# Performance work log

Measured on AMD Instinct MI355X. Metric: run time of the kernel, lower is better.

The kernel has to match this reference:

```python
import jax, jax.numpy as jnp
import numpy as np

S, D, M, K, H = 4096, 768, 1024, 32, 8
DH = D // H  # 96
CTX = 10
EPS_LN = 1e-5
EPS_COS = 1e-8


def setup_inputs() -> dict:
    key = jax.random.key(0)
    ks = jax.random.split(key, 30)
    sc = 0.02
    n = lambda k, shp: jax.random.normal(k, shp, jnp.float32) * sc
    inp = {
        "text_embeddings": jax.random.normal(ks[0], (1, S, D), jnp.float32),
        "candidate_embeddings": jax.random.normal(ks[1], (M, K, D), jnp.float32),
        "mention_starts": jax.random.randint(ks[2], (M,), 0, S - 16),
        "span_lengths": jax.random.randint(ks[3], (M,), 0, 8),
        # relik_reader: Linear(2D->D), ReLU, Linear(D->1)
        "relik_w1": n(ks[4], (2 * D, D)), "relik_b1": jnp.zeros((D,), jnp.float32),
        "relik_w2": n(ks[5], (D, 1)), "relik_b2": jnp.zeros((1,), jnp.float32),
        # TransformerEncoderLayer (post-norm, relu, nhead=8, ffn=4D)
        "wq": n(ks[6], (D, D)), "bq": jnp.zeros((D,), jnp.float32),
        "wk": n(ks[7], (D, D)), "bk": jnp.zeros((D,), jnp.float32),
        "wv": n(ks[8], (D, D)), "bv": jnp.zeros((D,), jnp.float32),
        "wo": n(ks[9], (D, D)), "bo": jnp.zeros((D,), jnp.float32),
        "ln1_g": jnp.ones((D,), jnp.float32), "ln1_b": jnp.zeros((D,), jnp.float32),
        "ffn_w1": n(ks[10], (D, 4 * D)), "ffn_b1": jnp.zeros((4 * D,), jnp.float32),
        "ffn_w2": n(ks[11], (4 * D, D)), "ffn_b2": jnp.zeros((D,), jnp.float32),
        "ln2_g": jnp.ones((D,), jnp.float32), "ln2_b": jnp.zeros((D,), jnp.float32),
        # unirel_interaction: Linear(2D->D), ReLU, Linear(D->D)
        "uni_w1": n(ks[12], (2 * D, D)), "uni_b1": jnp.zeros((D,), jnp.float32),
        "uni_w2": n(ks[13], (D, D)), "uni_b2": jnp.zeros((D,), jnp.float32),
    }
    return inp


def _ln(x, g, b):
    mu = jnp.mean(x, -1, keepdims=True)
    var = jnp.mean(jnp.square(x - mu), -1, keepdims=True)
    return (x - mu) * jax.lax.rsqrt(var + EPS_LN) * g + b


def reference(text_embeddings, candidate_embeddings, mention_starts, span_lengths,
              relik_w1, relik_b1, relik_w2, relik_b2,
              wq, bq, wk, bk, wv, bv, wo, bo,
              ln1_g, ln1_b, ffn_w1, ffn_b1, ffn_w2, ffn_b2, ln2_g, ln2_b,
              uni_w1, uni_b1, uni_w2, uni_b2):
    txt = text_embeddings[0]                               # [S, D]
    seq = txt.shape[0]
    csum = jnp.concatenate([jnp.zeros((1, txt.shape[1]), txt.dtype),
                            jnp.cumsum(txt, axis=0)], axis=0)  # [S+1, D]
    ends = mention_starts + span_lengths
    # mean over [start, end] inclusive
    m_len = (span_lengths + 1).astype(txt.dtype)
    mention = (csum[ends + 1] - csum[mention_starts]) / m_len[:, None]  # [M, D]
    # context mean over [c_start, c_end) exclusive, as in original slicing
    c_start = jnp.maximum(0, mention_starts - CTX)
    c_end = jnp.minimum(seq - 1, ends + CTX)
    ctx = (csum[c_end] - csum[c_start]) / (c_end - c_start).astype(txt.dtype)[:, None]

    cand = candidate_embeddings                            # [M, K, D]
    mk = jnp.broadcast_to(mention[:, None, :], cand.shape) # [M, K, D]

    # relik score: MLP on [mention; candidate]
    cat_mc = jnp.concatenate([mk, cand], axis=-1)          # [M, K, 2D]
    h = jax.nn.relu(cat_mc @ relik_w1 + relik_b1)
    relik = (h @ relik_w2 + relik_b2)[..., 0]              # [M, K]

    # 2-token transformer encoder layer over stack([mention, candidate])
    x = jnp.stack([mk, cand], axis=2)                      # [M, K, 2, D]
    q = (x @ wq + bq).reshape(M, K, 2, H, DH)
    k_ = (x @ wk + bk).reshape(M, K, 2, H, DH)
    v = (x @ wv + bv).reshape(M, K, 2, H, DH)
    scores = jnp.einsum("mkqhd,mkvhd->mkhqv", q, k_) / jnp.sqrt(jnp.float32(DH))
    attn = jax.nn.softmax(scores, axis=-1)
    o = jnp.einsum("mkhqv,mkvhd->mkqhd", attn, v).reshape(M, K, 2, D)
    x1 = _ln(x + (o @ wo + bo), ln1_g, ln1_b)
    f = jax.nn.relu(x1 @ ffn_w1 + ffn_b1) @ ffn_w2 + ffn_b2
    x2 = _ln(x1 + f, ln2_g, ln2_b)                         # [M, K, 2, D]
    e0, e1 = x2[..., 0, :], x2[..., 1, :]
    n0 = jnp.maximum(jnp.linalg.norm(e0, axis=-1), EPS_COS)
    n1 = jnp.maximum(jnp.linalg.norm(e1, axis=-1), EPS_COS)
    atg = jnp.sum(e0 * e1, axis=-1) / (n0 * n1)            # [M, K]

    # unirel: MLP on [context; candidate], sigmoid of mean
    ck = jnp.broadcast_to(ctx[:, None, :], cand.shape)
    cat_cc = jnp.concatenate([ck, cand], axis=-1)
    inter = jax.nn.relu(cat_cc @ uni_w1 + uni_b1) @ uni_w2 + uni_b2
    unirel = jax.nn.sigmoid(jnp.mean(inter, axis=-1))      # [M, K]

    return jnp.stack([relik, atg, unirel], axis=0)         # [3, M, K]
```

## Files before the change

### kernel.cpp

```cpp
#include <hip/hip_runtime.h>
#include <math.h>

#define S_LEN 4096
#define D_DIM 768
#define M_CNT 1024
#define K_CNT 32
#define MK_CNT 32768
#define DH_DIM 96
#define CTX_W 10

typedef __bf16 bf16_t;
typedef bf16_t bf16x8 __attribute__((ext_vector_type(8)));
typedef float f32x4 __attribute__((ext_vector_type(4)));
typedef float f32x16 __attribute__((ext_vector_type(16)));
typedef int i32x4 __attribute__((ext_vector_type(4)));
typedef int i32x8 __attribute__((ext_vector_type(8)));

__device__ __forceinline__ float block_reduce_sum(float v, float* sbuf) {
#pragma unroll
    for (int off = 32; off; off >>= 1) v += __shfl_down(v, off);
    __syncthreads();
    int wave = threadIdx.x >> 6;
    int lane = threadIdx.x & 63;
    if (lane == 0) sbuf[wave] = v;
    __syncthreads();
    return sbuf[0] + sbuf[1] + sbuf[2] + sbuf[3];
}

__device__ __forceinline__ float wave_sum(float v) {
#pragma unroll
    for (int off = 32; off; off >>= 1) v += __shfl_down(v, off);
    return __shfl(v, 0);
}

__device__ __forceinline__ unsigned char to_fp8(float v) {
    return (unsigned char)(__builtin_amdgcn_cvt_pk_fp8_f32(v, v, 0, false) & 0xff);
}

template<int OUT_BF16, int RELU>
__global__ __launch_bounds__(256, 2) void gemm_mfma(
    const bf16_t* __restrict__ A, const bf16_t* __restrict__ Bt,
    const float* __restrict__ bias, void* __restrict__ C,
    int Kd, int N, int nx, int ny)
{
    __shared__ bf16_t As[128 * 64];
    __shared__ bf16_t Bs[128 * 64];
    const int tid = threadIdx.x;
    const int w = tid >> 6, l = tid & 63;
    int per = 8 * nx;
    int g = blockIdx.x / per, rr = blockIdx.x % per;
    int gs = ny - g * 8; if (gs > 8) gs = 8;
    const int row0 = (g * 8 + rr % gs) * 128, col0 = (rr / gs) * 128;

    const int srow = w * 8 + (l >> 3);
    const int gchunk = (l & 7) ^ ((l >> 3) & 7);
    const bf16_t* gA = A + (size_t)(row0 + srow) * Kd + gchunk * 8;
    const bf16_t* gB = Bt + (size_t)(col0 + srow) * Kd + gchunk * 8;

    const int wm = w >> 1, wn = w & 1;
    f32x4 acc[4][4] = {};

    for (int k0 = 0; k0 < Kd; k0 += 64) {
#pragma unroll
        for (int c = 0; c < 4; ++c) {
            __builtin_amdgcn_global_load_lds(
                (const __attribute__((address_space(1))) void*)(gA + (size_t)(c * 32) * Kd + k0),
                (__attribute__((address_space(3))) void*)(As + (c * 256 + w * 64) * 8), 16, 0, 0);
            __builtin_amdgcn_global_load_lds(
                (const __attribute__((address_space(1))) void*)(gB + (size_t)(c * 32) * Kd + k0),
                (__attribute__((address_space(3))) void*)(Bs + (c * 256 + w * 64) * 8), 16, 0, 0);
        }
        __syncthreads();
#pragma unroll
        for (int ks = 0; ks < 2; ++ks) {
            bf16x8 af[4], bfr[4];
#pragma unroll
            for (int i = 0; i < 4; ++i) {
                int arow = wm * 64 + i * 16 + (l & 15);
                int slot = (ks * 4 + (l >> 4)) ^ (l & 7);
                af[i] = *(const bf16x8*)(As + arow * 64 + slot * 8);
                int brow = wn * 64 + i * 16 + (l & 15);
                bfr[i] = *(const bf16x8*)(Bs + brow * 64 + slot * 8);
            }
#pragma unroll
            for (int i = 0; i < 4; ++i)
#pragma unroll
                for (int j = 0; j < 4; ++j)
                    acc[i][j] = __builtin_amdgcn_mfma_f32_16x16x32_bf16(af[i], bfr[j], acc[i][j], 0, 0, 0);
        }
        __syncthreads();
    }

#pragma unroll
    for (int i = 0; i < 4; ++i) {
        int row = row0 + wm * 64 + i * 16 + (l >> 4) * 4;
#pragma unroll
        for (int j = 0; j < 4; ++j) {
            int col = col0 + wn * 64 + j * 16 + (l & 15);
            float bv = bias ? bias[col] : 0.f;
#pragma unroll
            for (int r = 0; r < 4; ++r) {
                float v = acc[i][j][r] + bv;
                if (RELU) v = fmaxf(v, 0.f);
                if (OUT_BF16) ((bf16_t*)C)[(size_t)(row + r) * N + col] = (bf16_t)v;
                else          ((float*)C)[(size_t)(row + r) * N + col] = v;
            }
        }
    }
}

static inline void launch_gemm(const bf16_t* A, const bf16_t* Bt, const float* bias, void* C,
                               int rows, int Kd, int N, bool relu, bool outbf, hipStream_t st) {
    int nx = N / 128, ny = rows / 128;
    dim3 grid(nx * ny);
    if (outbf) {
        if (relu) gemm_mfma<1, 1><<<grid, 256, 0, st>>>(A, Bt, bias, C, Kd, N, nx, ny);
        else      gemm_mfma<1, 0><<<grid, 256, 0, st>>>(A, Bt, bias, C, Kd, N, nx, ny);
    } else {
        if (relu) gemm_mfma<0, 1><<<grid, 256, 0, st>>>(A, Bt, bias, C, Kd, N, nx, ny);
        else      gemm_mfma<0, 0><<<grid, 256, 0, st>>>(A, Bt, bias, C, Kd, N, nx, ny);
    }
}

template<int OMODE, int RELU, int RESID>
__global__ __launch_bounds__(256, 2) void gemm_fp8(
    const unsigned char* __restrict__ A, const unsigned char* __restrict__ Bt,
    const float* __restrict__ bias, void* __restrict__ C,
    const bf16_t* __restrict__ resid,
    int Kd, int N, int nx, int ny)
{
    __shared__ unsigned char As[128 * 128];
    __shared__ unsigned char Bs[128 * 128];
    const int tid = threadIdx.x;
    const int w = tid >> 6, l = tid & 63;
    int per = 8 * nx;
    int g = blockIdx.x / per, rrb = blockIdx.x % per;
    int gs = ny - g * 8; if (gs > 8) gs = 8;
    const int row0 = (g * 8 + rrb % gs) * 128, col0 = (rrb / gs) * 128;
    const int wm = w >> 1, wn = w & 1;
    const int SA = 0x7F7F7F7F;

    const int srow = w * 8 + (l >> 3);
    const int gch = (l & 7) ^ ((l >> 3) & 7);
    const unsigned char* gA = A + (size_t)(row0 + srow) * Kd + gch * 16;
    const unsigned char* gB = Bt + (size_t)(col0 + srow) * Kd + gch * 16;

    f32x16 acc[2][2] = {};

    for (int k0 = 0; k0 < Kd; k0 += 128) {
#pragma unroll
        for (int q = 0; q < 4; ++q) {
            __builtin_amdgcn_global_load_lds(
                (const __attribute__((address_space(1))) void*)(gA + (size_t)(q * 32) * Kd + k0),
                (__attribute__((address_space(3))) void*)(As + (q * 256 + w * 64) * 16), 16, 0, 0);
            __builtin_amdgcn_global_load_lds(
                (const __attribute__((address_space(1))) void*)(gB + (size_t)(q * 32) * Kd + k0),
                (__attribute__((address_space(3))) void*)(Bs + (q * 256 + w * 64) * 16), 16, 0, 0);
        }
        __syncthreads();
#pragma unroll
        for (int s = 0; s < 2; ++s) {
            i32x8 af[2], bfr[2];
            int cb = s * 4 + ((l >> 5) << 1);
#pragma unroll
            for (int i = 0; i < 2; ++i) {
                int row = wm * 64 + i * 32 + (l & 31);
                int sl0 = cb ^ (row & 7);
                int sl1 = (cb + 1) ^ (row & 7);
                i32x4 lo = *(const i32x4*)(As + (row * 8 + sl0) * 16);
                i32x4 hi = *(const i32x4*)(As + (row * 8 + sl1) * 16);
                i32x8 a;
                a[0] = lo[0]; a[1] = lo[1]; a[2] = lo[2]; a[3] = lo[3];
                a[4] = hi[0]; a[5] = hi[1]; a[6] = hi[2]; a[7] = hi[3];
                af[i] = a;
                int colr = wn * 64 + i * 32 + (l & 31);
                int tl0 = cb ^ (colr & 7);
                int tl1 = (cb + 1) ^ (colr & 7);
                lo = *(const i32x4*)(Bs + (colr * 8 + tl0) * 16);
                hi = *(const i32x4*)(Bs + (colr * 8 + tl1) * 16);
                i32x8 b;
                b[0] = lo[0]; b[1] = lo[1]; b[2] = lo[2]; b[3] = lo[3];
                b[4] = hi[0]; b[5] = hi[1]; b[6] = hi[2]; b[7] = hi[3];
                bfr[i] = b;
            }
#pragma unroll
            for (int i = 0; i < 2; ++i)
#pragma unroll
                for (int j = 0; j < 2; ++j)
                    acc[i][j] = __builtin_amdgcn_mfma_scale_f32_32x32x64_f8f6f4(
                        af[i], bfr[j], acc[i][j], 0, 0, 0, SA, 0, SA);
        }
        __syncthreads();
    }

#pragma unroll
    for (int i = 0; i < 2; ++i) {
        int rbase = row0 + wm * 64 + i * 32 + 4 * (l >> 5);
#pragma unroll
        for (int j = 0; j < 2; ++j) {
            int col = col0 + wn * 64 + j * 32 + (l & 31);
            float bv = bias ? bias[col] : 0.f;
#pragma unroll
            for (int reg = 0; reg < 16; ++reg) {
                int row = rbase + (reg & 3) + 8 * (reg >> 2);
                float v = acc[i][j][reg] + bv;
                if (RESID) v += (float)resid[(size_t)row * N + col];
                if (RELU) v = fmaxf(v, 0.f);
                if (OMODE == 1)
                    ((unsigned char*)C)[(size_t)row * N + col] = to_fp8(v);
                else if (OMODE == 2)
                    ((bf16_t*)C)[(size_t)row * N + col] = (bf16_t)v;
                else
                    ((float*)C)[(size_t)row * N + col] = v;
            }
        }
    }
}

template<int OMODE, int RELU, int RESID>
static inline void launch_fp8_t(const unsigned char* A, const unsigned char* Bt, const float* bias,
                                void* C, const bf16_t* resid, int rows, int Kd, int N, hipStream_t st) {
    int nx = N / 128, ny = rows / 128;
    gemm_fp8<OMODE, RELU, RESID><<<dim3(nx * ny), 256, 0, st>>>(A, Bt, bias, C, resid, Kd, N, nx, ny);
}

__global__ __launch_bounds__(256) void transpose_bf16(
    const float* __restrict__ W, bf16_t* __restrict__ Wt, int Kd, int N)
{
    __shared__ float t[32][33];
    int bx = blockIdx.x * 32, by = blockIdx.y * 32;
    int x = threadIdx.x & 31, y = threadIdx.x >> 5;
#pragma unroll
    for (int yy = y; yy < 32; yy += 8) t[yy][x] = W[(size_t)(by + yy) * N + bx + x];
    __syncthreads();
#pragma unroll
    for (int yy = y; yy < 32; yy += 8) Wt[(size_t)(bx + yy) * Kd + by + x] = (bf16_t)t[x][yy];
}

__global__ __launch_bounds__(256) void transpose_fp8(
    const float* __restrict__ W, unsigned char* __restrict__ Wt, int Kd, int N)
{
    __shared__ float t[32][33];
    int bx = blockIdx.x * 32, by = blockIdx.y * 32;
    int x = threadIdx.x & 31, y = threadIdx.x >> 5;
#pragma unroll
    for (int yy = y; yy < 32; yy += 8) t[yy][x] = W[(size_t)(by + yy) * N + bx + x];
    __syncthreads();
    int xg = threadIdx.x & 7, yo = threadIdx.x >> 3;
    int lo = __builtin_amdgcn_cvt_pk_fp8_f32(t[xg * 4 + 0][yo], t[xg * 4 + 1][yo], 0, false);
    int both = __builtin_amdgcn_cvt_pk_fp8_f32(t[xg * 4 + 2][yo], t[xg * 4 + 3][yo], lo, true);
    *(int*)(Wt + (size_t)(bx + yo) * Kd + by + xg * 4) = both;
}

__global__ __launch_bounds__(256) void cvt_cand(
    const float* __restrict__ x, bf16_t* __restrict__ yb,
    unsigned char* __restrict__ yq, int n4)
{
    int i = blockIdx.x * 256 + threadIdx.x;
    if (i < n4) {
        float4 v = ((const float4*)x)[i];
        bf16_t o4[4] = {(bf16_t)v.x, (bf16_t)v.y, (bf16_t)v.z, (bf16_t)v.w};
        ((uint2*)yb)[i] = *(uint2*)o4;
        int lo = __builtin_amdgcn_cvt_pk_fp8_f32(v.x, v.y, 0, false);
        int both = __builtin_amdgcn_cvt_pk_fp8_f32(v.z, v.w, lo, true);
        ((int*)yq)[i] = both;
    }
}

__global__ __launch_bounds__(256) void pack_bias(
    const float* __restrict__ bq, const float* __restrict__ bk,
    const float* __restrict__ bv, float* __restrict__ o)
{
    int i = blockIdx.x * 256 + threadIdx.x;
    if (i < 768) { o[i] = bq[i]; o[i + 768] = bk[i]; o[i + 1536] = bv[i]; }
}

__global__ __launch_bounds__(256) void spans_kernel(
    const float* __restrict__ txt, const int* __restrict__ starts,
    const int* __restrict__ lens, float* __restrict__ mention,
    unsigned char* __restrict__ mentionq, bf16_t* __restrict__ mentionb,
    bf16_t* __restrict__ ctxb)
{
    int m = blockIdx.x;
    int st = starts[m], ln = lens[m];
    int en = st + ln;
    int cs = st - CTX_W; if (cs < 0) cs = 0;
    int ce = en + CTX_W; if (ce > S_LEN - 1) ce = S_LEN - 1;
    int c = threadIdx.x;
    float s0 = 0.f, s1 = 0.f, s2 = 0.f;
    for (int r = st; r <= en; ++r) {
        const float* tr = txt + (size_t)r * D_DIM;
        s0 += tr[c]; s1 += tr[c + 256]; s2 += tr[c + 512];
    }
    float inv = 1.f / (float)(ln + 1);
    float v0 = s0 * inv, v1 = s1 * inv, v2 = s2 * inv;
    float* mp = mention + (size_t)m * D_DIM;
    bf16_t* mb = mentionb + (size_t)m * D_DIM;
    unsigned char* mq = mentionq + (size_t)m * D_DIM;
    mp[c] = v0; mp[c + 256] = v1; mp[c + 512] = v2;
    mb[c] = (bf16_t)v0; mb[c + 256] = (bf16_t)v1; mb[c + 512] = (bf16_t)v2;
    mq[c] = to_fp8(v0); mq[c + 256] = to_fp8(v1); mq[c + 512] = to_fp8(v2);

    s0 = 0.f; s1 = 0.f; s2 = 0.f;
    for (int r = cs; r < ce; ++r) {
        const float* tr = txt + (size_t)r * D_DIM;
        s0 += tr[c]; s1 += tr[c + 256]; s2 += tr[c + 512];
    }
    inv = 1.f / (float)(ce - cs);
    bf16_t* cp = ctxb + (size_t)m * D_DIM;
    cp[c] = (bf16_t)(s0 * inv); cp[c + 256] = (bf16_t)(s1 * inv); cp[c + 512] = (bf16_t)(s2 * inv);
}

__global__ __launch_bounds__(256) void w2bar_kernel(
    const float* __restrict__ uni_w2, const float* __restrict__ uni_b2,
    float* __restrict__ w2bar, float* __restrict__ b2bar)
{
    __shared__ float sbuf[4];
    int d = blockIdx.x;
    float s = 0.f;
    if (d < D_DIM) {
        for (int j = threadIdx.x; j < D_DIM; j += 256) s += uni_w2[(size_t)d * D_DIM + j];
        s = block_reduce_sum(s, sbuf);
        if (threadIdx.x == 0) w2bar[d] = s * (1.f / (float)D_DIM);
    } else {
        for (int j = threadIdx.x; j < D_DIM; j += 256) s += uni_b2[j];
        s = block_reduce_sum(s, sbuf);
        if (threadIdx.x == 0) *b2bar = s * (1.f / (float)D_DIM);
    }
}

__global__ __launch_bounds__(512) void attn_kernel(
    const bf16_t* __restrict__ qkvm, const bf16_t* __restrict__ qkvc,
    unsigned char* __restrict__ o, int g0)
{
    int lc = blockIdx.x;
    int gg = g0 + lc;
    int m = gg >> 5;
    int h = threadIdx.x >> 6;
    int lane = threadIdx.x & 63;
    const bf16_t* bm = qkvm + (size_t)m * 2304 + h * DH_DIM;
    const bf16_t* bc = qkvc + (size_t)lc * 2304 + h * DH_DIM;

    float s00 = 0.f, s01 = 0.f, s10 = 0.f, s11 = 0.f;
    for (int d = lane; d < DH_DIM; d += 64) {
        float qmv = (float)bm[d], kmv = (float)bm[d + 768];
        float qcv = (float)bc[d], kcv = (float)bc[d + 768];
        s00 += qmv * kmv; s01 += qmv * kcv; s10 += qcv * kmv; s11 += qcv * kcv;
    }
#pragma unroll
    for (int off = 32; off; off >>= 1) {
        s00 += __shfl_down(s00, off); s01 += __shfl_down(s01, off);
        s10 += __shfl_down(s10, off); s11 += __shfl_down(s11, off);
    }
    s00 = __shfl(s00, 0); s01 = __shfl(s01, 0);
    s10 = __shfl(s10, 0); s11 = __shfl(s11, 0);
    const float sc = 0.1020620726159658f;
    s00 *= sc; s01 *= sc; s10 *= sc; s11 *= sc;
    float m0 = fmaxf(s00, s01), m1 = fmaxf(s10, s11);
    float e00 = expf(s00 - m0), e01 = expf(s01 - m0);
    float e10 = expf(s10 - m1), e11 = expf(s11 - m1);
    float i0 = 1.f / (e00 + e01), i1 = 1.f / (e10 + e11);
    float a00 = e00 * i0, a01 = e01 * i0, a10 = e10 * i1, a11 = e11 * i1;

    unsigned char* o0 = o + ((size_t)lc * 2) * D_DIM + h * DH_DIM;
    unsigned char* o1 = o0 + D_DIM;
    for (int d = lane; d < DH_DIM; d += 64) {
        float vmv = (float)bm[d + 1536], vcv = (float)bc[d + 1536];
        o0[d] = to_fp8(a00 * vmv + a01 * vcv);
        o1[d] = to_fp8(a10 * vmv + a11 * vcv);
    }
}

__global__ __launch_bounds__(256) void ln1_kernel(
    const bf16_t* __restrict__ x1pre, const float* __restrict__ mention,
    const bf16_t* __restrict__ candb, const float* __restrict__ g,
    const float* __restrict__ b, bf16_t* __restrict__ x1f,
    unsigned char* __restrict__ x1q, int g0)
{
    int w = threadIdx.x >> 6, l = threadIdx.x & 63;
    int r = blockIdx.x * 4 + w;
    int lc = r >> 1, pos = r & 1;
    int gg = g0 + lc, m = gg >> 5;
    float v[12];
    const bf16_t* pr = x1pre + (size_t)r * D_DIM;
    if (pos) {
        const bf16_t* xr = candb + (size_t)gg * D_DIM;
#pragma unroll
        for (int i = 0; i < 12; ++i) { int j = l + i * 64; v[i] = (float)xr[j] + (float)pr[j]; }
    } else {
        const float* xr = mention + (size_t)m * D_DIM;
#pragma unroll
        for (int i = 0; i < 12; ++i) { int j = l + i * 64; v[i] = xr[j] + (float)pr[j]; }
    }
    float s = 0.f;
#pragma unroll
    for (int i = 0; i < 12; ++i) s += v[i];
    float mu = wave_sum(s) * (1.f / (float)D_DIM);
    float vv = 0.f;
#pragma unroll
    for (int i = 0; i < 12; ++i) { float d = v[i] - mu; vv += d * d; }
    float var = wave_sum(vv) * (1.f / (float)D_DIM);
    float inv = rsqrtf(var + 1e-5f);
    bf16_t* fp = x1f + (size_t)r * D_DIM;
    unsigned char* qp = x1q + (size_t)r * D_DIM;
#pragma unroll
    for (int i = 0; i < 12; ++i) {
        int j = l + i * 64;
        float o = (v[i] - mu) * inv * g[j] + b[j];
        fp[j] = (bf16_t)o;
        qp[j] = to_fp8(o);
    }
}

__global__ __launch_bounds__(256) void heads_kernel(
    const bf16_t* __restrict__ y,
    const float* __restrict__ g2, const float* __restrict__ b2g,
    const float* __restrict__ Ar, const float* __restrict__ Au,
    const bf16_t* __restrict__ ru, const float* __restrict__ rw2,
    const float* __restrict__ rb2, const float* __restrict__ w2bar,
    const float* __restrict__ b2bar, float* __restrict__ out, int g0)
{
    int w = threadIdx.x >> 6, l = threadIdx.x & 63;
    int lc = blockIdx.x * 4 + w;
    int gg = g0 + lc, m = gg >> 5;
    const bf16_t* y0 = y + (size_t)(2 * lc) * D_DIM;
    const bf16_t* y1 = y0 + D_DIM;
    float v0[12], v1[12];
    float s0 = 0.f, s1 = 0.f;
#pragma unroll
    for (int i = 0; i < 12; ++i) {
        int j = l + i * 64;
        v0[i] = (float)y0[j]; v1[i] = (float)y1[j];
        s0 += v0[i]; s1 += v1[i];
    }
    float mu0 = wave_sum(s0) * (1.f / (float)D_DIM);
    float mu1 = wave_sum(s1) * (1.f / (float)D_DIM);
    float q0 = 0.f, q1 = 0.f;
#pragma unroll
    for (int i = 0; i < 12; ++i) {
        float d0 = v0[i] - mu0, d1 = v1[i] - mu1;
        q0 += d0 * d0; q1 += d1 * d1;
    }
    float inv0 = rsqrtf(wave_sum(q0) * (1.f / (float)D_DIM) + 1e-5f);
    float inv1 = rsqrtf(wave_sum(q1) * (1.f / (float)D_DIM) + 1e-5f);

    const float* ar = Ar + (size_t)m * D_DIM;
    const float* au = Au + (size_t)m * D_DIM;
    const bf16_t* br = ru + (size_t)lc * 1536;
    const bf16_t* bu = br + 768;

    float dd = 0.f, aa = 0.f, bb = 0.f, rs = 0.f, us = 0.f;
#pragma unroll
    for (int i = 0; i < 12; ++i) {
        int j = l + i * 64;
        float e0 = (v0[i] - mu0) * inv0 * g2[j] + b2g[j];
        float e1 = (v1[i] - mu1) * inv1 * g2[j] + b2g[j];
        dd += e0 * e1; aa += e0 * e0; bb += e1 * e1;
        rs += fmaxf(ar[j] + (float)br[j], 0.f) * rw2[j];
        us += fmaxf(au[j] + (float)bu[j], 0.f) * w2bar[j];
    }
    dd = wave_sum(dd); aa = wave_sum(aa); bb = wave_sum(bb);
    rs = wave_sum(rs); us = wave_sum(us);
    if (l == 0) {
        float n0 = fmaxf(sqrtf(aa), 1e-8f);
        float n1 = fmaxf(sqrtf(bb), 1e-8f);
        out[MK_CNT + gg] = dd / (n0 * n1);
        out[gg] = rs + rb2[0];
        float z = us + *b2bar;
        out[2 * MK_CNT + gg] = 1.f / (1.f + expf(-z));
    }
}

extern "C" void kernel_launch(void* const* d_in, const int* in_sizes, int n_in,
                              void* d_out, int out_size, void* d_ws, size_t ws_size,
                              hipStream_t stream) {
    const float* text     = (const float*)d_in[0];
    const float* cand     = (const float*)d_in[1];
    const int*   starts   = (const int*)d_in[2];
    const int*   lens     = (const int*)d_in[3];
    const float* relik_w1 = (const float*)d_in[4];
    const float* relik_b1 = (const float*)d_in[5];
    const float* relik_w2 = (const float*)d_in[6];
    const float* relik_b2 = (const float*)d_in[7];
    const float* wq = (const float*)d_in[8];
    const float* bq = (const float*)d_in[9];
    const float* wk = (const float*)d_in[10];
    const float* bk = (const float*)d_in[11];
    const float* wv = (const float*)d_in[12];
    const float* bv = (const float*)d_in[13];
    const float* wo = (const float*)d_in[14];
    const float* bo = (const float*)d_in[15];
    const float* ln1_g = (const float*)d_in[16];
    const float* ln1_b = (const float*)d_in[17];
    const float* ffn_w1 = (const float*)d_in[18];
    const float* ffn_b1 = (const float*)d_in[19];
    const float* ffn_w2 = (const float*)d_in[20];
    const float* ffn_b2 = (const float*)d_in[21];
    const float* ln2_g = (const float*)d_in[22];
    const float* ln2_b = (const float*)d_in[23];
    const float* uni_w1 = (const float*)d_in[24];
    const float* uni_b1 = (const float*)d_in[25];
    const float* uni_w2 = (const float*)d_in[26];
    const float* uni_b2 = (const float*)d_in[27];
    float* out = (float*)d_out;

    const size_t MD = (size_t)M_CNT * D_DIM;
    const size_t DD = (size_t)D_DIM * D_DIM;

    size_t fixed_f = 26500000;
    int NC = 32768;
    while (NC > 128 && (fixed_f + (size_t)NC * 6528) * 4 > ws_size) NC >>= 1;
    const size_t NCD = (size_t)NC * D_DIM;

    float* p = (float*)d_ws;
    float* mention = p; p += MD;
    float* Ar      = p; p += MD;
    float* Au      = p; p += MD;
    float* bqkv    = p; p += 2304;
    float* w2bar   = p; p += 768;
    float* b2bar   = p; p += 64;
    bf16_t* mentionb = (bf16_t*)p; p += MD / 2;
    bf16_t* ctxb     = (bf16_t*)p; p += MD / 2;
    unsigned char* mentionq = (unsigned char*)p; p += MD / 4;
    bf16_t* qkvm     = (bf16_t*)p; p += (size_t)M_CNT * 2304 / 2;
    bf16_t* relikAT  = (bf16_t*)p; p += DD / 2;
    bf16_t* uniAT    = (bf16_t*)p; p += DD / 2;
    bf16_t* wruT     = (bf16_t*)p; p += 2 * DD / 2;
    unsigned char* wqkvq = (unsigned char*)p; p += 3 * DD / 4;
    unsigned char* woq   = (unsigned char*)p; p += DD / 4;
    unsigned char* w1q = (unsigned char*)p; p += (size_t)3072 * 768 / 4;
    unsigned char* w2q = (unsigned char*)p; p += (size_t)3072 * 768 / 4;
    bf16_t* candb    = (bf16_t*)p; p += (size_t)MK_CNT * D_DIM / 2;
    unsigned char* candq = (unsigned char*)p; p += (size_t)MK_CNT * D_DIM / 4;
    bf16_t* qkvcb = (bf16_t*)p; p += (size_t)NC * 2304 / 2;
    bf16_t* rucb  = (bf16_t*)p; p += (size_t)NC * 1536 / 2;
    unsigned char* obuf = (unsigned char*)p; p += 2 * NCD / 4;
    bf16_t* x1pre = (bf16_t*)p; p += 2 * NCD / 2;
    bf16_t* x1f   = (bf16_t*)p; p += 2 * NCD / 2;
    bf16_t* x2f   = (bf16_t*)p; p += 2 * NCD / 2;
    unsigned char* x1q = (unsigned char*)p; p += 2 * NCD / 4;
    unsigned char* hb  = (unsigned char*)p; p += (size_t)2 * NC * 3072 / 4;

    dim3 t768(768 / 32, 768 / 32);
    transpose_fp8<<<t768, 256, 0, stream>>>(wq, wqkvq, 768, 768);
    transpose_fp8<<<t768, 256, 0, stream>>>(wk, wqkvq + DD, 768, 768);
    transpose_fp8<<<t768, 256, 0, stream>>>(wv, wqkvq + 2 * DD, 768, 768);
    transpose_fp8<<<t768, 256, 0, stream>>>(wo, woq, 768, 768);
    transpose_bf16<<<t768, 256, 0, stream>>>(relik_w1 + DD, wruT, 768, 768);
    transpose_bf16<<<t768, 256, 0, stream>>>(uni_w1 + DD, wruT + DD, 768, 768);
    transpose_bf16<<<t768, 256, 0, stream>>>(relik_w1, relikAT, 768, 768);
    transpose_bf16<<<t768, 256, 0, stream>>>(uni_w1, uniAT, 768, 768);
    transpose_fp8<<<dim3(3072 / 32, 768 / 32), 256, 0, stream>>>(ffn_w1, w1q, 768, 3072);
    transpose_fp8<<<dim3(768 / 32, 3072 / 32), 256, 0, stream>>>(ffn_w2, w2q, 3072, 768);
    pack_bias<<<3, 256, 0, stream>>>(bq, bk, bv, bqkv);
    w2bar_kernel<<<D_DIM + 1, 256, 0, stream>>>(uni_w2, uni_b2, w2bar, b2bar);
    cvt_cand<<<(MK_CNT * D_DIM / 4 + 255) / 256, 256, 0, stream>>>(cand, candb, candq, MK_CNT * D_DIM / 4);

    spans_kernel<<<M_CNT, 256, 0, stream>>>(text, starts, lens, mention, mentionq, mentionb, ctxb);
    launch_fp8_t<2, 0, 0>(mentionq, wqkvq, bqkv, qkvm, nullptr, M_CNT, 768, 2304, stream);
    launch_gemm(mentionb, relikAT, relik_b1, Ar, M_CNT, 768, 768, false, false, stream);
    launch_gemm(ctxb, uniAT, uni_b1, Au, M_CNT, 768, 768, false, false, stream);

    int nch = MK_CNT / NC;
    for (int c = 0; c < nch; ++c) {
        int g0 = c * NC;
        launch_fp8_t<2, 0, 0>(candq + (size_t)g0 * D_DIM, wqkvq, bqkv, qkvcb, nullptr, NC, 768, 2304, stream);
        launch_gemm(candb + (size_t)g0 * D_DIM, wruT, nullptr, rucb, NC, 768, 1536, false, true, stream);

        attn_kernel<<<NC, 512, 0, stream>>>(qkvm, qkvcb, obuf, g0);

        launch_fp8_t<2, 0, 0>(obuf, woq, bo, x1pre, nullptr, 2 * NC, 768, 768, stream);
        ln1_kernel<<<2 * NC / 4, 256, 0, stream>>>(x1pre, mention, candb,
                                                   ln1_g, ln1_b, x1f, x1q, g0);

        launch_fp8_t<1, 1, 0>(x1q, w1q, ffn_b1, hb, nullptr, 2 * NC, 768, 3072, stream);
        launch_fp8_t<2, 0, 1>(hb, w2q, ffn_b2, x2f, x1f, 2 * NC, 3072, 768, stream);

        heads_kernel<<<NC / 4, 256, 0, stream>>>(x2f, ln2_g, ln2_b, Ar, Au, rucb,
                                                 relik_w2, relik_b2, w2bar, b2bar, out, g0);
    }
}
```

Measured before the change: 1.209 ms.

## Enlarge FP8 GEMM row tile, vectorize attention loads, alias workspace buffers

```diff
diff --git a/kernel.cpp b/kernel.cpp
--- a/kernel.cpp
+++ b/kernel.cpp
@@ -35,6 +35,12 @@
 
 __device__ __forceinline__ unsigned char to_fp8(float v) {
     return (unsigned char)(__builtin_amdgcn_cvt_pk_fp8_f32(v, v, 0, false) & 0xff);
+}
+
+__device__ __forceinline__ void ld2(const bf16_t* p, float& a, float& b) {
+    ushort2 u = *(const ushort2*)p;
+    a = __uint_as_float((unsigned)u.x << 16);
+    b = __uint_as_float((unsigned)u.y << 16);
 }
 
 template<int OUT_BF16, int RELU>
@@ -129,14 +135,14 @@
     const bf16_t* __restrict__ resid,
     int Kd, int N, int nx, int ny)
 {
-    __shared__ unsigned char As[128 * 128];
+    __shared__ unsigned char As[256 * 128];
     __shared__ unsigned char Bs[128 * 128];
     const int tid = threadIdx.x;
     const int w = tid >> 6, l = tid & 63;
     int per = 8 * nx;
     int g = blockIdx.x / per, rrb = blockIdx.x % per;
     int gs = ny - g * 8; if (gs > 8) gs = 8;
-    const int row0 = (g * 8 + rrb % gs) * 128, col0 = (rrb / gs) * 128;
+    const int row0 = (g * 8 + rrb % gs) * 256, col0 = (rrb / gs) * 128;
     const int wm = w >> 1, wn = w & 1;
     const int SA = 0x7F7F7F7F;
 
@@ -145,26 +151,27 @@
     const unsigned char* gA = A + (size_t)(row0 + srow) * Kd + gch * 16;
     const unsigned char* gB = Bt + (size_t)(col0 + srow) * Kd + gch * 16;
 
-    f32x16 acc[2][2] = {};
+    f32x16 acc[4][2] = {};
 
     for (int k0 = 0; k0 < Kd; k0 += 128) {
 #pragma unroll
-        for (int q = 0; q < 4; ++q) {
+        for (int q = 0; q < 8; ++q)
             __builtin_amdgcn_global_load_lds(
                 (const __attribute__((address_space(1))) void*)(gA + (size_t)(q * 32) * Kd + k0),
                 (__attribute__((address_space(3))) void*)(As + (q * 256 + w * 64) * 16), 16, 0, 0);
+#pragma unroll
+        for (int q = 0; q < 4; ++q)
             __builtin_amdgcn_global_load_lds(
                 (const __attribute__((address_space(1))) void*)(gB + (size_t)(q * 32) * Kd + k0),
                 (__attribute__((address_space(3))) void*)(Bs + (q * 256 + w * 64) * 16), 16, 0, 0);
-        }
         __syncthreads();
 #pragma unroll
         for (int s = 0; s < 2; ++s) {
-            i32x8 af[2], bfr[2];
             int cb = s * 4 + ((l >> 5) << 1);
-#pragma unroll
-            for (int i = 0; i < 2; ++i) {
-                int row = wm * 64 + i * 32 + (l & 31);
+            i32x8 af[4], bfr[2];
+#pragma unroll
+            for (int i = 0; i < 4; ++i) {
+                int row = wm * 128 + i * 32 + (l & 31);
                 int sl0 = cb ^ (row & 7);
                 int sl1 = (cb + 1) ^ (row & 7);
                 i32x4 lo = *(const i32x4*)(As + (row * 8 + sl0) * 16);
@@ -173,18 +180,21 @@
                 a[0] = lo[0]; a[1] = lo[1]; a[2] = lo[2]; a[3] = lo[3];
                 a[4] = hi[0]; a[5] = hi[1]; a[6] = hi[2]; a[7] = hi[3];
                 af[i] = a;
-                int colr = wn * 64 + i * 32 + (l & 31);
+            }
+#pragma unroll
+            for (int j = 0; j < 2; ++j) {
+                int colr = wn * 64 + j * 32 + (l & 31);
                 int tl0 = cb ^ (colr & 7);
                 int tl1 = (cb + 1) ^ (colr & 7);
-                lo = *(const i32x4*)(Bs + (colr * 8 + tl0) * 16);
-                hi = *(const i32x4*)(Bs + (colr * 8 + tl1) * 16);
+                i32x4 lo = *(const i32x4*)(Bs + (colr * 8 + tl0) * 16);
+                i32x4 hi = *(const i32x4*)(Bs + (colr * 8 + tl1) * 16);
                 i32x8 b;
                 b[0] = lo[0]; b[1] = lo[1]; b[2] = lo[2]; b[3] = lo[3];
                 b[4] = hi[0]; b[5] = hi[1]; b[6] = hi[2]; b[7] = hi[3];
-                bfr[i] = b;
+                bfr[j] = b;
             }
 #pragma unroll
-            for (int i = 0; i < 2; ++i)
+            for (int i = 0; i < 4; ++i)
 #pragma unroll
                 for (int j = 0; j < 2; ++j)
                     acc[i][j] = __builtin_amdgcn_mfma_scale_f32_32x32x64_f8f6f4(
@@ -194,8 +204,8 @@
     }
 
 #pragma unroll
-    for (int i = 0; i < 2; ++i) {
-        int rbase = row0 + wm * 64 + i * 32 + 4 * (l >> 5);
+    for (int i = 0; i < 4; ++i) {
+        int rbase = row0 + wm * 128 + i * 32 + 4 * (l >> 5);
 #pragma unroll
         for (int j = 0; j < 2; ++j) {
             int col = col0 + wn * 64 + j * 32 + (l & 31);
@@ -220,7 +230,7 @@
 template<int OMODE, int RELU, int RESID>
 static inline void launch_fp8_t(const unsigned char* A, const unsigned char* Bt, const float* bias,
                                 void* C, const bf16_t* resid, int rows, int Kd, int N, hipStream_t st) {
-    int nx = N / 128, ny = rows / 128;
+    int nx = N / 128, ny = rows / 256;
     gemm_fp8<OMODE, RELU, RESID><<<dim3(nx * ny), 256, 0, st>>>(A, Bt, bias, C, resid, Kd, N, nx, ny);
 }
 
@@ -342,10 +352,17 @@
     const bf16_t* bc = qkvc + (size_t)lc * 2304 + h * DH_DIM;
 
     float s00 = 0.f, s01 = 0.f, s10 = 0.f, s11 = 0.f;
-    for (int d = lane; d < DH_DIM; d += 64) {
-        float qmv = (float)bm[d], kmv = (float)bm[d + 768];
-        float qcv = (float)bc[d], kcv = (float)bc[d + 768];
-        s00 += qmv * kmv; s01 += qmv * kcv; s10 += qcv * kmv; s11 += qcv * kcv;
+    int d = lane * 2;
+    if (lane < 48) {
+        float qm0, qm1, km0, km1, qc0, qc1, kc0, kc1;
+        ld2(bm + d, qm0, qm1);
+        ld2(bm + 768 + d, km0, km1);
+        ld2(bc + d, qc0, qc1);
+        ld2(bc + 768 + d, kc0, kc1);
+        s00 = qm0 * km0 + qm1 * km1;
+        s01 = qm0 * kc0 + qm1 * kc1;
+        s10 = qc0 * km0 + qc1 * km1;
+        s11 = qc0 * kc0 + qc1 * kc1;
     }
 #pragma unroll
     for (int off = 32; off; off >>= 1) {
@@ -364,10 +381,14 @@
 
     unsigned char* o0 = o + ((size_t)lc * 2) * D_DIM + h * DH_DIM;
     unsigned char* o1 = o0 + D_DIM;
-    for (int d = lane; d < DH_DIM; d += 64) {
-        float vmv = (float)bm[d + 1536], vcv = (float)bc[d + 1536];
-        o0[d] = to_fp8(a00 * vmv + a01 * vcv);
-        o1[d] = to_fp8(a10 * vmv + a11 * vcv);
+    if (lane < 48) {
+        float vm0, vm1, vc0, vc1;
+        ld2(bm + 1536 + d, vm0, vm1);
+        ld2(bc + 1536 + d, vc0, vc1);
+        unsigned r0 = __builtin_amdgcn_cvt_pk_fp8_f32(a00 * vm0 + a01 * vc0, a00 * vm1 + a01 * vc1, 0, false);
+        unsigned r1 = __builtin_amdgcn_cvt_pk_fp8_f32(a10 * vm0 + a11 * vc0, a10 * vm1 + a11 * vc1, 0, false);
+        *(unsigned short*)(o0 + d) = (unsigned short)(r0 & 0xffff);
+        *(unsigned short*)(o1 + d) = (unsigned short)(r1 & 0xffff);
     }
 }
 
@@ -509,7 +530,7 @@
 
     size_t fixed_f = 26500000;
     int NC = 32768;
-    while (NC > 128 && (fixed_f + (size_t)NC * 6528) * 4 > ws_size) NC >>= 1;
+    while (NC > 256 && (fixed_f + (size_t)NC * 4224) * 4 > ws_size) NC >>= 1;
     const size_t NCD = (size_t)NC * D_DIM;
 
     float* p = (float*)d_ws;
@@ -532,14 +553,18 @@
     unsigned char* w2q = (unsigned char*)p; p += (size_t)3072 * 768 / 4;
     bf16_t* candb    = (bf16_t*)p; p += (size_t)MK_CNT * D_DIM / 2;
     unsigned char* candq = (unsigned char*)p; p += (size_t)MK_CNT * D_DIM / 4;
-    bf16_t* qkvcb = (bf16_t*)p; p += (size_t)NC * 2304 / 2;
+
+    bf16_t* qkvcb = (bf16_t*)p;
+    bf16_t* x1f   = (bf16_t*)p;
+    unsigned char* x1q = (unsigned char*)(x1f + 2 * NCD);
+    p += (size_t)NC * 2304 / 2;
     bf16_t* rucb  = (bf16_t*)p; p += (size_t)NC * 1536 / 2;
-    unsigned char* obuf = (unsigned char*)p; p += 2 * NCD / 4;
-    bf16_t* x1pre = (bf16_t*)p; p += 2 * NCD / 2;
-    bf16_t* x1f   = (bf16_t*)p; p += 2 * NCD / 2;
-    bf16_t* x2f   = (bf16_t*)p; p += 2 * NCD / 2;
-    unsigned char* x1q = (unsigned char*)p; p += 2 * NCD / 4;
-    unsigned char* hb  = (unsigned char*)p; p += (size_t)2 * NC * 3072 / 4;
+    bf16_t* x1pre = (bf16_t*)p;
+    bf16_t* x2f   = x1pre;
+    p += NCD;
+    unsigned char* hb   = (unsigned char*)p;
+    unsigned char* obuf = hb;
+    p += (size_t)NC * 1536;
 
     dim3 t768(768 / 32, 768 / 32);
     transpose_fp8<<<t768, 256, 0, stream>>>(wq, wqkvq, 768, 768);
```

Measured after the change: 1.177 ms. 2.7% less time.
